# Kernel tuning notes

Hardware: AMD Instinct MI355X
Metric: run time of the kernel (lower is better)

Reference implementation:

```python
import jax, jax.numpy as jnp
import numpy as np

H, C, OC, WIN = 12, 768, 768, 4
HD = C // H  # 64
B, T = 4, 1024


def setup_inputs() -> dict:
    key = jax.random.key(0)
    ks = jax.random.split(key, 8)
    s = C ** -0.5  # xavier-ish scale for 1x1 convs
    rel_s = HD ** -0.5
    return {
        "x": jax.random.normal(ks[0], (B, C, T), jnp.float32),
        "c": jax.random.normal(ks[1], (B, C, T), jnp.float32),
        "mask": jnp.ones((B, 1, T, T), jnp.float32),
        "wq": jax.random.normal(ks[2], (C, C), jnp.float32) * s,
        "bq": jnp.zeros((C,), jnp.float32),
        "wk": jax.random.normal(ks[3], (C, C), jnp.float32) * s,
        "bk": jnp.zeros((C,), jnp.float32),
        "wv": jax.random.normal(ks[4], (C, C), jnp.float32) * s,
        "bv": jnp.zeros((C,), jnp.float32),
        "wo": jax.random.normal(ks[5], (OC, C), jnp.float32) * s,
        "bo": jnp.zeros((OC,), jnp.float32),
        "emb_rel_k": jax.random.normal(ks[6], (H, 2 * WIN + 1, HD), jnp.float32) * rel_s,
        "emb_rel_v": jax.random.normal(ks[7], (H, 2 * WIN + 1, HD), jnp.float32) * rel_s,
    }


def _conv1x1(x, w, b):
    # Conv1d(kernel_size=1): pointwise linear over channels. x:(b,c,t) w:(o,c)
    return jnp.einsum('oc,bct->bot', w, x) + b[None, :, None]


def _get_rel_emb(emb, t):
    pad = max(t - WIN, 0)
    start = max(WIN + 1 - t, 0)
    emb = jnp.pad(emb, ((0, 0), (pad, pad), (0, 0)))
    return emb[:, start:start + 2 * t - 1, :]


def _rel_to_abs(x):
    # (b,h,t,2t-1) -> (b,h,t,t) via the pad/reshape skew trick
    b, h, t, _ = x.shape
    x = jnp.pad(x, ((0, 0), (0, 0), (0, 0), (0, 1))).reshape(b, h, 2 * t * t)
    x = jnp.pad(x, ((0, 0), (0, 0), (0, t - 1))).reshape(b, h, t + 1, 2 * t - 1)
    return x[:, :, :t, t - 1:]


def _abs_to_rel(x):
    # (b,h,t,t) -> (b,h,t,2t-1) via inverse skew trick
    b, h, t, _ = x.shape
    x = jnp.pad(x, ((0, 0), (0, 0), (0, 0), (0, t - 1))).reshape(b, h, t * (2 * t - 1))
    x = jnp.pad(x, ((0, 0), (0, 0), (t, 0))).reshape(b, h, t, 2 * t)
    return x[:, :, :, 1:]


def reference(x, c, mask, wq, bq, wk, bk, wv, bv, wo, bo, emb_rel_k, emb_rel_v):
    b, _, t = x.shape
    scale = HD ** -0.5
    # (b,c,t) -> (b,h,t,hd)
    q = _conv1x1(x, wq, bq).reshape(b, H, HD, t).transpose(0, 1, 3, 2)
    k = _conv1x1(c, wk, bk).reshape(b, H, HD, t).transpose(0, 1, 3, 2)
    v = _conv1x1(c, wv, bv).reshape(b, H, HD, t).transpose(0, 1, 3, 2)
    scores = jnp.einsum('bhqd,bhkd->bhqk', q, k) * scale  # (b,h,t,t)
    rel_k = _get_rel_emb(emb_rel_k, t)                    # (h,2t-1,d)
    rel_logits = jnp.einsum('bhtd,hmd->bhtm', q, rel_k)   # (b,h,t,2t-1)
    scores = scores + _rel_to_abs(rel_logits) * scale
    scores = jnp.where(mask == 0, jnp.float32(-1e4), scores)
    attn = jax.nn.softmax(scores, axis=-1)
    out = jnp.einsum('bhqk,bhkd->bhqd', attn, v)
    rel_v = _get_rel_emb(emb_rel_v, t)
    out = out + jnp.einsum('bhtm,hmd->bhtd', _abs_to_rel(attn), rel_v)
    out = out.transpose(0, 1, 3, 2).reshape(b, C, t)      # (b,c,t)
    return _conv1x1(out, wo, bo)
```

## Files before the change

kernel.cpp:

```cpp
#include <hip/hip_runtime.h>
#include <stdint.h>
#include <stddef.h>

#define B_ 4
#define T_ 1024
#define C_ 768
#define H_ 12

typedef __attribute__((ext_vector_type(4))) float f32x4;
typedef __attribute__((ext_vector_type(8))) short s16x8;
typedef __attribute__((ext_vector_type(4))) float float4v;

typedef const __attribute__((address_space(1))) uint32_t ga_u32;
typedef __attribute__((address_space(3))) uint32_t lds_u32;

__device__ __forceinline__ float bf2f(uint16_t u) {
    union { uint32_t u; float f; } cv; cv.u = ((uint32_t)u) << 16; return cv.f;
}
__device__ __forceinline__ uint16_t f2bf(float f) {
    union { float f; uint32_t u; } cv; cv.f = f;
    uint32_t u = cv.u;
    return (uint16_t)((u + 0x7FFFu + ((u >> 16) & 1u)) >> 16);
}
__device__ __forceinline__ void gload16(const uint16_t* g, uint16_t* l) {
    __builtin_amdgcn_global_load_lds((ga_u32*)g, (lds_u32*)l, 16, 0, 0);
}

__global__ void transpose_bf16_kernel(const float* __restrict__ x,
                                      const float* __restrict__ c,
                                      uint16_t* __restrict__ xT,
                                      uint16_t* __restrict__ cT) {
    __shared__ float tile[32][33];
    const int which = blockIdx.z;
    const int b = blockIdx.y;
    const int t0 = (blockIdx.x % (T_ / 32)) * 32;
    const int c0 = (blockIdx.x / (T_ / 32)) * 32;
    const float* src = (which ? c : x) + (size_t)b * C_ * T_;
    uint16_t* dst = (which ? cT : xT) + (size_t)b * T_ * C_;
    const int lj = threadIdx.x & 31, li = threadIdx.x >> 5;
    #pragma unroll
    for (int i = li; i < 32; i += 8)
        tile[i][lj] = src[(size_t)(c0 + i) * T_ + t0 + lj];
    __syncthreads();
    #pragma unroll
    for (int i = li; i < 32; i += 8)
        dst[(size_t)(t0 + i) * C_ + c0 + lj] = f2bf(tile[lj][i]);
}

__global__ void convert_weights_kernel(const float* __restrict__ wq,
                                       const float* __restrict__ wk,
                                       const float* __restrict__ wv,
                                       const float* __restrict__ wo,
                                       uint16_t* __restrict__ out) {
    const int which = blockIdx.y;
    const float* w = (which == 0) ? wq : (which == 1) ? wk : (which == 2) ? wv : wo;
    uint16_t* dst = out + (size_t)which * C_ * C_;
    const int i = (blockIdx.x * 256 + threadIdx.x) * 4;
    float4v v = *(const float4v*)(w + i);
    uint32_t lo = (uint32_t)f2bf(v[0]) | ((uint32_t)f2bf(v[1]) << 16);
    uint32_t hi = (uint32_t)f2bf(v[2]) | ((uint32_t)f2bf(v[3]) << 16);
    uint32_t* d32 = (uint32_t*)(dst + i);
    d32[0] = lo; d32[1] = hi;
}

__global__ void mask_bits_kernel(const float* __restrict__ mask,
                                 uint32_t* __restrict__ bits) {
    const size_t i = (size_t)blockIdx.x * 256 + threadIdx.x;
    const float m = mask[i];
    unsigned long long bal = __ballot(m != 0.0f);
    const int lane = threadIdx.x & 63;
    if (lane == 0)       bits[i >> 5] = (uint32_t)bal;
    else if (lane == 32) bits[i >> 5] = (uint32_t)(bal >> 32);
}

template <bool OPROJ>
__global__ __launch_bounds__(256, 2)
void gemm_kernel(const uint16_t* __restrict__ xT, const uint16_t* __restrict__ cT,
                 const uint16_t* __restrict__ wb,
                 const float* __restrict__ bq, const float* __restrict__ bk,
                 const float* __restrict__ bv, const float* __restrict__ bo,
                 const uint16_t* __restrict__ attT,
                 uint16_t* __restrict__ Qb, uint16_t* __restrict__ Kb,
                 uint16_t* __restrict__ Vb, float* __restrict__ outp) {
    const int tid = threadIdx.x;
    const int z = blockIdx.z;

    const uint16_t* A; const uint16_t* Bm; const float* bias;
    uint16_t* Cb = nullptr; float* Cf = nullptr;
    int N, ldc; bool bias_col;
    if (!OPROJ) {
        const int bat = z & 3, which = z >> 2;
        if (which == 0) {
            A = xT + (size_t)bat * T_ * C_; Bm = wb;                bias = bq;
            Cb = Qb + (size_t)bat * T_ * C_; N = C_; ldc = C_; bias_col = true;
        } else if (which == 1) {
            A = cT + (size_t)bat * T_ * C_; Bm = wb + 1 * C_ * C_;  bias = bk;
            Cb = Kb + (size_t)bat * T_ * C_; N = C_; ldc = C_; bias_col = true;
        } else {
            A = wb + 2 * (size_t)C_ * C_;   Bm = cT + (size_t)(z & 3) * T_ * C_; bias = bv;
            Cb = Vb + (size_t)bat * C_ * T_; N = T_; ldc = T_; bias_col = false;
        }
    } else {
        A = wb + 3 * (size_t)C_ * C_; Bm = attT + (size_t)z * T_ * C_; bias = bo;
        Cf = outp + (size_t)z * C_ * T_; N = T_; ldc = T_; bias_col = false;
    }
    const int tn_cnt = N / 128;
    const int tm = blockIdx.x / tn_cnt, tn = blockIdx.x % tn_cnt;
    const int row0 = tm * 128, col0 = tn * 128;

    __shared__ uint16_t As[128 * 64];
    __shared__ uint16_t Bs[128 * 64];

    const int w = tid >> 6, l = tid & 63;
    const int wr = w & 1, wc = w >> 1;

    const f32x4 zz = {0.f, 0.f, 0.f, 0.f};
    f32x4 acc[4][4];
    #pragma unroll
    for (int i = 0; i < 4; ++i)
        #pragma unroll
        for (int j = 0; j < 4; ++j) acc[i][j] = zz;

    const int sr = tid >> 3, sp = tid & 7;

    for (int kt = 0; kt < 12; ++kt) {
        const int k0 = kt * 64;
        #pragma unroll
        for (int it = 0; it < 4; ++it) {
            const int row = it * 32 + sr;
            const int cch = sp ^ (row & 7);
            gload16(A + (size_t)(row0 + row) * 768 + k0 + cch * 8, &As[row * 64 + sp * 8]);
        }
        #pragma unroll
        for (int it = 0; it < 4; ++it) {
            const int row = it * 32 + sr;
            const int cch = sp ^ (row & 7);
            gload16(Bm + (size_t)(col0 + row) * 768 + k0 + cch * 8, &Bs[row * 64 + sp * 8]);
        }
        __syncthreads();

        #pragma unroll
        for (int kk = 0; kk < 2; ++kk) {
            s16x8 af[4], bf[4];
            #pragma unroll
            for (int i = 0; i < 4; ++i) {
                const int arow = wr * 64 + i * 16 + (l & 15);
                const int ach = (kk * 4 + (l >> 4)) ^ (arow & 7);
                af[i] = *(const s16x8*)(&As[arow * 64 + ach * 8]);
                const int brow = wc * 64 + i * 16 + (l & 15);
                const int bch = (kk * 4 + (l >> 4)) ^ (brow & 7);
                bf[i] = *(const s16x8*)(&Bs[brow * 64 + bch * 8]);
            }
            #pragma unroll
            for (int i = 0; i < 4; ++i)
                #pragma unroll
                for (int j = 0; j < 4; ++j)
                    acc[i][j] = __builtin_amdgcn_mfma_f32_16x16x32_bf16(af[i], bf[j], acc[i][j], 0, 0, 0);
        }
        __syncthreads();
    }

    #pragma unroll
    for (int i = 0; i < 4; ++i) {
        const int rowb = row0 + wr * 64 + i * 16 + ((l >> 4) * 4);
        #pragma unroll
        for (int j = 0; j < 4; ++j) {
            const int col = col0 + wc * 64 + j * 16 + (l & 15);
            const float bc = bias_col ? bias[col] : 0.f;
            #pragma unroll
            for (int r = 0; r < 4; ++r) {
                const int row = rowb + r;
                const float v = acc[i][j][r] + (bias_col ? bc : bias[row]);
                if (!OPROJ) Cb[(size_t)row * ldc + col] = f2bf(v);
                else        Cf[(size_t)row * ldc + col] = v;
            }
        }
    }
}

__global__ __launch_bounds__(256, 2)
void attn_kernel(const uint16_t* __restrict__ Qb, const uint16_t* __restrict__ Kb,
                 const uint16_t* __restrict__ Vb, const uint32_t* __restrict__ mbits,
                 const float* __restrict__ emb_k, const float* __restrict__ emb_v,
                 uint16_t* __restrict__ attT) {
    const int i0 = blockIdx.x * 64;
    const int h = blockIdx.y, b = blockIdx.z;
    const int tid = threadIdx.x, w = tid >> 6, l = tid & 63;
    const float scale = 0.125f;

    __shared__ uint16_t Ks[64 * 64];
    __shared__ uint16_t Vs[64 * 64];
    __shared__ uint16_t Ps[64 * 72];
    __shared__ float rk[64 * 9];
    __shared__ float sband[64 * 9];

    s16x8 qf[2];
    {
        const int row = i0 + w * 16 + (l & 15);
        const uint16_t* qp = Qb + ((size_t)(b * T_ + row)) * C_ + h * 64 + (l >> 4) * 8;
        qf[0] = *(const s16x8*)(qp);
        qf[1] = *(const s16x8*)(qp + 32);
    }
    for (int t = tid; t < 64 * 9; t += 256) {
        const int rr = t % 9, row = t / 9;
        const uint16_t* qp = Qb + ((size_t)(b * T_ + i0 + row)) * C_ + h * 64;
        const float* ep = emb_k + ((size_t)h * 9 + rr) * 64;
        float s = 0.f;
        #pragma unroll
        for (int d = 0; d < 64; ++d) s += bf2f(qp[d]) * ep[d];
        rk[t] = s * scale;
        sband[t] = -1e30f;
    }
    __syncthreads();

    float m[4], lsum[4];
    const f32x4 zz = {0.f, 0.f, 0.f, 0.f};
    f32x4 oacc[4] = {zz, zz, zz, zz};
    #pragma unroll
    for (int r = 0; r < 4; ++r) { m[r] = -1e30f; lsum[r] = 0.f; }

    const uint16_t* Kbase = Kb + (size_t)b * T_ * C_ + h * 64;
    const uint16_t* Vbase = Vb + (size_t)b * C_ * T_ + (size_t)(h * 64) * T_;
    const uint32_t* mrow = mbits + (size_t)b * T_ * 32;
    const int sr = tid >> 3, sp = tid & 7;

    for (int jt = 0; jt < 16; ++jt) {
        const int j0 = jt * 64;
        #pragma unroll
        for (int it = 0; it < 2; ++it) {
            const int row = it * 32 + sr;
            const int cch = sp ^ (row & 7);
            gload16(Kbase + (size_t)(j0 + row) * C_ + cch * 8, &Ks[row * 64 + sp * 8]);
        }
        #pragma unroll
        for (int it = 0; it < 2; ++it) {
            const int row = it * 32 + sr;
            const int cch = sp ^ (row & 7);
            gload16(Vbase + (size_t)row * T_ + j0 + cch * 8, &Vs[row * 64 + sp * 8]);
        }
        __syncthreads();

        float sv[4][4];
        #pragma unroll
        for (int tn = 0; tn < 4; ++tn) {
            f32x4 s = zz;
            #pragma unroll
            for (int kk = 0; kk < 2; ++kk) {
                const int krow = tn * 16 + (l & 15);
                const int kch = (kk * 4 + (l >> 4)) ^ (krow & 7);
                s16x8 kf = *(const s16x8*)(&Ks[krow * 64 + kch * 8]);
                s = __builtin_amdgcn_mfma_f32_16x16x32_bf16(qf[kk], kf, s, 0, 0, 0);
            }
            #pragma unroll
            for (int r = 0; r < 4; ++r) {
                const int iloc = w * 16 + (l >> 4) * 4 + r;
                const int i = i0 + iloc;
                const int j = j0 + tn * 16 + (l & 15);
                float sc = s[r] * scale;
                const int rr = j - i + 3;
                const bool band = (rr >= 0) && (rr < 9);
                if (band) sc += rk[iloc * 9 + rr];
                const uint32_t mw = mrow[(size_t)i * 32 + (j >> 5)];
                if (!((mw >> (j & 31)) & 1u)) sc = -1e4f;
                if (band) sband[iloc * 9 + rr] = sc;
                sv[tn][r] = sc;
            }
        }

        #pragma unroll
        for (int r = 0; r < 4; ++r) {
            float rm = fmaxf(fmaxf(sv[0][r], sv[1][r]), fmaxf(sv[2][r], sv[3][r]));
            rm = fmaxf(rm, __shfl_xor(rm, 1));
            rm = fmaxf(rm, __shfl_xor(rm, 2));
            rm = fmaxf(rm, __shfl_xor(rm, 4));
            rm = fmaxf(rm, __shfl_xor(rm, 8));
            const float mn = fmaxf(m[r], rm);
            const float alpha = __expf(m[r] - mn);
            m[r] = mn;
            float rs = 0.f;
            #pragma unroll
            for (int tn = 0; tn < 4; ++tn) {
                const float p = __expf(sv[tn][r] - mn);
                sv[tn][r] = p;
                rs += p;
            }
            rs += __shfl_xor(rs, 1);
            rs += __shfl_xor(rs, 2);
            rs += __shfl_xor(rs, 4);
            rs += __shfl_xor(rs, 8);
            lsum[r] = lsum[r] * alpha + rs;
            #pragma unroll
            for (int td = 0; td < 4; ++td) oacc[td][r] *= alpha;
        }

        #pragma unroll
        for (int tn = 0; tn < 4; ++tn)
            #pragma unroll
            for (int r = 0; r < 4; ++r) {
                const int prow = w * 16 + (l >> 4) * 4 + r;
                Ps[prow * 72 + tn * 16 + (l & 15)] = f2bf(sv[tn][r]);
            }
        __syncthreads();

        #pragma unroll
        for (int ks = 0; ks < 2; ++ks) {
            const int prow = w * 16 + (l & 15);
            s16x8 pf = *(const s16x8*)(&Ps[prow * 72 + ks * 32 + (l >> 4) * 8]);
            #pragma unroll
            for (int td = 0; td < 4; ++td) {
                const int vrow = td * 16 + (l & 15);
                const int vch = (ks * 4 + (l >> 4)) ^ (vrow & 7);
                s16x8 vf = *(const s16x8*)(&Vs[vrow * 64 + vch * 8]);
                oacc[td] = __builtin_amdgcn_mfma_f32_16x16x32_bf16(pf, vf, oacc[td], 0, 0, 0);
            }
        }
        __syncthreads();
    }

    float invl[4];
    #pragma unroll
    for (int r = 0; r < 4; ++r) invl[r] = 1.f / lsum[r];
    float ab[4][9];
    #pragma unroll
    for (int r = 0; r < 4; ++r) {
        const int iloc = w * 16 + (l >> 4) * 4 + r;
        #pragma unroll
        for (int rr = 0; rr < 9; ++rr)
            ab[r][rr] = __expf(sband[iloc * 9 + rr] - m[r]) * invl[r];
    }
    #pragma unroll
    for (int td = 0; td < 4; ++td) {
        const int d = td * 16 + (l & 15);
        const float* ev = emb_v + (size_t)h * 9 * 64 + d;
        #pragma unroll
        for (int r = 0; r < 4; ++r) {
            float v = oacc[td][r] * invl[r];
            #pragma unroll
            for (int rr = 0; rr < 9; ++rr) v += ab[r][rr] * ev[rr * 64];
            const int i = i0 + w * 16 + (l >> 4) * 4 + r;
            attT[((size_t)(b * T_ + i)) * C_ + h * 64 + d] = f2bf(v);
        }
    }
}

extern "C" void kernel_launch(void* const* d_in, const int* in_sizes, int n_in,
                              void* d_out, int out_size, void* d_ws, size_t ws_size,
                              hipStream_t stream) {
    const float* x    = (const float*)d_in[0];
    const float* c    = (const float*)d_in[1];
    const float* mask = (const float*)d_in[2];
    const float* wq   = (const float*)d_in[3];
    const float* bq   = (const float*)d_in[4];
    const float* wk   = (const float*)d_in[5];
    const float* bk   = (const float*)d_in[6];
    const float* wv   = (const float*)d_in[7];
    const float* bv   = (const float*)d_in[8];
    const float* wo   = (const float*)d_in[9];
    const float* bo   = (const float*)d_in[10];
    const float* ek   = (const float*)d_in[11];
    const float* ev   = (const float*)d_in[12];
    float* out = (float*)d_out;

    uint8_t* ws = (uint8_t*)d_ws;
    size_t off = 0;
    auto alloc = [&](size_t bytes) {
        uint8_t* p = ws + off;
        off += (bytes + 255) & ~(size_t)255;
        return p;
    };
    uint16_t* xT   = (uint16_t*)alloc((size_t)B_ * T_ * C_ * 2);
    uint16_t* cT   = (uint16_t*)alloc((size_t)B_ * T_ * C_ * 2);
    uint16_t* wb   = (uint16_t*)alloc((size_t)4 * C_ * C_ * 2);
    uint16_t* Qb   = (uint16_t*)alloc((size_t)B_ * T_ * C_ * 2);
    uint16_t* Kb   = (uint16_t*)alloc((size_t)B_ * T_ * C_ * 2);
    uint16_t* Vb   = (uint16_t*)alloc((size_t)B_ * C_ * T_ * 2);
    uint16_t* attT = (uint16_t*)alloc((size_t)B_ * T_ * C_ * 2);
    uint32_t* mbits = (uint32_t*)alloc((size_t)B_ * T_ * 32 * 4);

    transpose_bf16_kernel<<<dim3(768, B_, 2), 256, 0, stream>>>(x, c, xT, cT);
    convert_weights_kernel<<<dim3(576, 4), 256, 0, stream>>>(wq, wk, wv, wo, wb);
    mask_bits_kernel<<<dim3((B_ * T_ * T_) / 256), 256, 0, stream>>>(mask, mbits);
    gemm_kernel<false><<<dim3(48, 1, 12), 256, 0, stream>>>(xT, cT, wb, bq, bk, bv, bo,
                                                            attT, Qb, Kb, Vb, out);
    attn_kernel<<<dim3(T_ / 64, H_, B_), 256, 0, stream>>>(Qb, Kb, Vb, mbits, ek, ev, attT);
    gemm_kernel<true><<<dim3(48, 1, 4), 256, 0, stream>>>(xT, cT, wb, bq, bk, bv, bo,
                                                          attT, Qb, Kb, Vb, out);
}
```

Before: 247.2 us.

## Double-buffer K/V tiles, fold softmax scale into Wq, skip mask/band work

Double-buffers the K/V LDS tiles so the next tile's global-to-LDS load is issued before computing the current one, and drops the per-tile barrier before the PV step. The attention scale and log2(e) are folded into the bf16 Wq weights and bias so the softmax can use exp2 without per-element scaling. Per-element mask checks are skipped when the block's mask is all ones, and relative-band work is limited to tiles that touch the band. The running max rescale is applied only when some row max increases. Together these cut ALU work and load latency in the attention loop, at the cost of more LDS and an extra mask pre-scan.

```diff
diff --git a/kernel.cpp b/kernel.cpp
--- a/kernel.cpp
+++ b/kernel.cpp
@@ -6,6 +6,8 @@
 #define T_ 1024
 #define C_ 768
 #define H_ 12
+#define QSCALE 0.18033688011112042f
+#define MASKPEN -14427.0f
 
 typedef __attribute__((ext_vector_type(4))) float f32x4;
 typedef __attribute__((ext_vector_type(8))) short s16x8;
@@ -54,11 +56,12 @@
                                        uint16_t* __restrict__ out) {
     const int which = blockIdx.y;
     const float* w = (which == 0) ? wq : (which == 1) ? wk : (which == 2) ? wv : wo;
+    const float sc = (which == 0) ? QSCALE : 1.0f;
     uint16_t* dst = out + (size_t)which * C_ * C_;
     const int i = (blockIdx.x * 256 + threadIdx.x) * 4;
     float4v v = *(const float4v*)(w + i);
-    uint32_t lo = (uint32_t)f2bf(v[0]) | ((uint32_t)f2bf(v[1]) << 16);
-    uint32_t hi = (uint32_t)f2bf(v[2]) | ((uint32_t)f2bf(v[3]) << 16);
+    uint32_t lo = (uint32_t)f2bf(v[0] * sc) | ((uint32_t)f2bf(v[1] * sc) << 16);
+    uint32_t hi = (uint32_t)f2bf(v[2] * sc) | ((uint32_t)f2bf(v[3] * sc) << 16);
     uint32_t* d32 = (uint32_t*)(dst + i);
     d32[0] = lo; d32[1] = hi;
 }
@@ -87,12 +90,13 @@
 
     const uint16_t* A; const uint16_t* Bm; const float* bias;
     uint16_t* Cb = nullptr; float* Cf = nullptr;
-    int N, ldc; bool bias_col;
+    int N, ldc; bool bias_col; float bscale = 1.0f;
     if (!OPROJ) {
         const int bat = z & 3, which = z >> 2;
         if (which == 0) {
             A = xT + (size_t)bat * T_ * C_; Bm = wb;                bias = bq;
             Cb = Qb + (size_t)bat * T_ * C_; N = C_; ldc = C_; bias_col = true;
+            bscale = QSCALE;
         } else if (which == 1) {
             A = cT + (size_t)bat * T_ * C_; Bm = wb + 1 * C_ * C_;  bias = bk;
             Cb = Kb + (size_t)bat * T_ * C_; N = C_; ldc = C_; bias_col = true;
@@ -166,7 +170,7 @@
         #pragma unroll
         for (int j = 0; j < 4; ++j) {
             const int col = col0 + wc * 64 + j * 16 + (l & 15);
-            const float bc = bias_col ? bias[col] : 0.f;
+            const float bc = bias_col ? bias[col] * bscale : 0.f;
             #pragma unroll
             for (int r = 0; r < 4; ++r) {
                 const int row = rowb + r;
@@ -186,13 +190,43 @@
     const int i0 = blockIdx.x * 64;
     const int h = blockIdx.y, b = blockIdx.z;
     const int tid = threadIdx.x, w = tid >> 6, l = tid & 63;
-    const float scale = 0.125f;
-
-    __shared__ uint16_t Ks[64 * 64];
-    __shared__ uint16_t Vs[64 * 64];
+
+    __shared__ uint16_t Ks[2][64 * 64];
+    __shared__ uint16_t Vs[2][64 * 64];
     __shared__ uint16_t Ps[64 * 72];
     __shared__ float rk[64 * 9];
     __shared__ float sband[64 * 9];
+    __shared__ int s_allones;
+
+    const uint16_t* Kbase = Kb + (size_t)b * T_ * C_ + h * 64;
+    const uint16_t* Vbase = Vb + (size_t)b * C_ * T_ + (size_t)(h * 64) * T_;
+    const uint32_t* mrow = mbits + (size_t)b * T_ * 32;
+    const int sr = tid >> 3, sp = tid & 7;
+
+    auto stage = [&](int jt, int buf) {
+        const int j0s = jt * 64;
+        #pragma unroll
+        for (int it = 0; it < 2; ++it) {
+            const int row = it * 32 + sr;
+            const int cch = sp ^ (row & 7);
+            gload16(Kbase + (size_t)(j0s + row) * C_ + cch * 8, &Ks[buf][row * 64 + sp * 8]);
+        }
+        #pragma unroll
+        for (int it = 0; it < 2; ++it) {
+            const int row = it * 32 + sr;
+            const int cch = sp ^ (row & 7);
+            gload16(Vbase + (size_t)row * T_ + j0s + cch * 8, &Vs[buf][row * 64 + sp * 8]);
+        }
+    };
+
+    stage(0, 0);
+
+    bool mok = true;
+    {
+        const uint32_t* mb = mrow + (size_t)i0 * 32;
+        #pragma unroll
+        for (int it = 0; it < 8; ++it) mok &= (mb[it * 256 + tid] == 0xFFFFFFFFu);
+    }
 
     s16x8 qf[2];
     {
@@ -203,15 +237,22 @@
     }
     for (int t = tid; t < 64 * 9; t += 256) {
         const int rr = t % 9, row = t / 9;
-        const uint16_t* qp = Qb + ((size_t)(b * T_ + i0 + row)) * C_ + h * 64;
+        const uint32_t* q32 = (const uint32_t*)(Qb + ((size_t)(b * T_ + i0 + row)) * C_ + h * 64);
         const float* ep = emb_k + ((size_t)h * 9 + rr) * 64;
         float s = 0.f;
         #pragma unroll
-        for (int d = 0; d < 64; ++d) s += bf2f(qp[d]) * ep[d];
-        rk[t] = s * scale;
+        for (int d2 = 0; d2 < 32; ++d2) {
+            const uint32_t u = q32[d2];
+            s += bf2f((uint16_t)u) * ep[2 * d2] + bf2f((uint16_t)(u >> 16)) * ep[2 * d2 + 1];
+        }
+        rk[t] = s;
         sband[t] = -1e30f;
     }
+    if (tid == 0) s_allones = 1;
     __syncthreads();
+    if (!mok) s_allones = 0;
+    __syncthreads();
+    const bool maskones = (s_allones != 0);
 
     float m[4], lsum[4];
     const f32x4 zz = {0.f, 0.f, 0.f, 0.f};
@@ -219,26 +260,12 @@
     #pragma unroll
     for (int r = 0; r < 4; ++r) { m[r] = -1e30f; lsum[r] = 0.f; }
 
-    const uint16_t* Kbase = Kb + (size_t)b * T_ * C_ + h * 64;
-    const uint16_t* Vbase = Vb + (size_t)b * C_ * T_ + (size_t)(h * 64) * T_;
-    const uint32_t* mrow = mbits + (size_t)b * T_ * 32;
-    const int sr = tid >> 3, sp = tid & 7;
+    const int iMin = i0 + w * 16, iMax = iMin + 15;
 
     for (int jt = 0; jt < 16; ++jt) {
+        const int cur = jt & 1;
+        if (jt < 15) stage(jt + 1, cur ^ 1);
         const int j0 = jt * 64;
-        #pragma unroll
-        for (int it = 0; it < 2; ++it) {
-            const int row = it * 32 + sr;
-            const int cch = sp ^ (row & 7);
-            gload16(Kbase + (size_t)(j0 + row) * C_ + cch * 8, &Ks[row * 64 + sp * 8]);
-        }
-        #pragma unroll
-        for (int it = 0; it < 2; ++it) {
-            const int row = it * 32 + sr;
-            const int cch = sp ^ (row & 7);
-            gload16(Vbase + (size_t)row * T_ + j0 + cch * 8, &Vs[row * 64 + sp * 8]);
-        }
-        __syncthreads();
 
         float sv[4][4];
         #pragma unroll
@@ -248,39 +275,77 @@
             for (int kk = 0; kk < 2; ++kk) {
                 const int krow = tn * 16 + (l & 15);
                 const int kch = (kk * 4 + (l >> 4)) ^ (krow & 7);
-                s16x8 kf = *(const s16x8*)(&Ks[krow * 64 + kch * 8]);
+                s16x8 kf = *(const s16x8*)(&Ks[cur][krow * 64 + kch * 8]);
                 s = __builtin_amdgcn_mfma_f32_16x16x32_bf16(qf[kk], kf, s, 0, 0, 0);
             }
             #pragma unroll
+            for (int r = 0; r < 4; ++r) sv[tn][r] = s[r];
+        }
+
+        const bool bandTile = (j0 <= iMax + 5) && (j0 + 63 >= iMin - 3);
+        if (bandTile) {
+            #pragma unroll
+            for (int tn = 0; tn < 4; ++tn)
+                #pragma unroll
+                for (int r = 0; r < 4; ++r) {
+                    const int iloc = w * 16 + (l >> 4) * 4 + r;
+                    const int rr = (j0 + tn * 16 + (l & 15)) - (i0 + iloc) + 3;
+                    if ((unsigned)rr < 9u) sv[tn][r] += rk[iloc * 9 + rr];
+                }
+        }
+        if (!maskones) {
+            #pragma unroll
             for (int r = 0; r < 4; ++r) {
-                const int iloc = w * 16 + (l >> 4) * 4 + r;
-                const int i = i0 + iloc;
-                const int j = j0 + tn * 16 + (l & 15);
-                float sc = s[r] * scale;
-                const int rr = j - i + 3;
-                const bool band = (rr >= 0) && (rr < 9);
-                if (band) sc += rk[iloc * 9 + rr];
-                const uint32_t mw = mrow[(size_t)i * 32 + (j >> 5)];
-                if (!((mw >> (j & 31)) & 1u)) sc = -1e4f;
-                if (band) sband[iloc * 9 + rr] = sc;
-                sv[tn][r] = sc;
-            }
-        }
-
+                const int i = i0 + w * 16 + (l >> 4) * 4 + r;
+                const uint32_t m0 = mrow[(size_t)i * 32 + (j0 >> 5)];
+                const uint32_t m1 = mrow[(size_t)i * 32 + (j0 >> 5) + 1];
+                #pragma unroll
+                for (int tn = 0; tn < 4; ++tn) {
+                    const uint32_t mw = (tn < 2) ? m0 : m1;
+                    const int bit = (tn * 16 + (l & 15)) & 31;
+                    if (!((mw >> bit) & 1u)) sv[tn][r] = MASKPEN;
+                }
+            }
+        }
+        if (bandTile) {
+            #pragma unroll
+            for (int tn = 0; tn < 4; ++tn)
+                #pragma unroll
+                for (int r = 0; r < 4; ++r) {
+                    const int iloc = w * 16 + (l >> 4) * 4 + r;
+                    const int rr = (j0 + tn * 16 + (l & 15)) - (i0 + iloc) + 3;
+                    if ((unsigned)rr < 9u) sband[iloc * 9 + rr] = sv[tn][r];
+                }
+        }
+
+        float rm[4];
         #pragma unroll
         for (int r = 0; r < 4; ++r) {
-            float rm = fmaxf(fmaxf(sv[0][r], sv[1][r]), fmaxf(sv[2][r], sv[3][r]));
-            rm = fmaxf(rm, __shfl_xor(rm, 1));
-            rm = fmaxf(rm, __shfl_xor(rm, 2));
-            rm = fmaxf(rm, __shfl_xor(rm, 4));
-            rm = fmaxf(rm, __shfl_xor(rm, 8));
-            const float mn = fmaxf(m[r], rm);
-            const float alpha = __expf(m[r] - mn);
-            m[r] = mn;
+            float v = fmaxf(fmaxf(sv[0][r], sv[1][r]), fmaxf(sv[2][r], sv[3][r]));
+            v = fmaxf(v, __shfl_xor(v, 1));
+            v = fmaxf(v, __shfl_xor(v, 2));
+            v = fmaxf(v, __shfl_xor(v, 4));
+            v = fmaxf(v, __shfl_xor(v, 8));
+            rm[r] = v;
+        }
+        const bool need = (rm[0] > m[0]) | (rm[1] > m[1]) | (rm[2] > m[2]) | (rm[3] > m[3]);
+        if (__any(need)) {
+            #pragma unroll
+            for (int r = 0; r < 4; ++r) {
+                const float mn = fmaxf(m[r], rm[r]);
+                const float alpha = exp2f(m[r] - mn);
+                m[r] = mn;
+                lsum[r] *= alpha;
+                #pragma unroll
+                for (int td = 0; td < 4; ++td) oacc[td][r] *= alpha;
+            }
+        }
+        #pragma unroll
+        for (int r = 0; r < 4; ++r) {
             float rs = 0.f;
             #pragma unroll
             for (int tn = 0; tn < 4; ++tn) {
-                const float p = __expf(sv[tn][r] - mn);
+                const float p = exp2f(sv[tn][r] - m[r]);
                 sv[tn][r] = p;
                 rs += p;
             }
@@ -288,9 +353,7 @@
             rs += __shfl_xor(rs, 2);
             rs += __shfl_xor(rs, 4);
             rs += __shfl_xor(rs, 8);
-            lsum[r] = lsum[r] * alpha + rs;
-            #pragma unroll
-            for (int td = 0; td < 4; ++td) oacc[td][r] *= alpha;
+            lsum[r] += rs;
         }
 
         #pragma unroll
@@ -300,7 +363,6 @@
                 const int prow = w * 16 + (l >> 4) * 4 + r;
                 Ps[prow * 72 + tn * 16 + (l & 15)] = f2bf(sv[tn][r]);
             }
-        __syncthreads();
 
         #pragma unroll
         for (int ks = 0; ks < 2; ++ks) {
@@ -310,7 +372,7 @@
             for (int td = 0; td < 4; ++td) {
                 const int vrow = td * 16 + (l & 15);
                 const int vch = (ks * 4 + (l >> 4)) ^ (vrow & 7);
-                s16x8 vf = *(const s16x8*)(&Vs[vrow * 64 + vch * 8]);
+                s16x8 vf = *(const s16x8*)(&Vs[cur][vrow * 64 + vch * 8]);
                 oacc[td] = __builtin_amdgcn_mfma_f32_16x16x32_bf16(pf, vf, oacc[td], 0, 0, 0);
             }
         }
@@ -326,7 +388,7 @@
         const int iloc = w * 16 + (l >> 4) * 4 + r;
         #pragma unroll
         for (int rr = 0; rr < 9; ++rr)
-            ab[r][rr] = __expf(sband[iloc * 9 + rr] - m[r]) * invl[r];
+            ab[r][rr] = exp2f(sband[iloc * 9 + rr] - m[r]) * invl[r];
     }
     #pragma unroll
     for (int td = 0; td < 4; ++td) {
```

Measured after the change: 254.1 us. 1.03x slower.
